# Kernel tuning notes

Hardware: AMD Instinct MI355X
Metric: run time of the kernel (lower is better)

## Reference

```python
import jax, jax.numpy as jnp
import numpy as np

N = 100000      # nodes
E = 1600000     # edges (avg degree 16)
DIN = 128       # input feature dim
DOUT = 64       # per-head output dim
H = 4           # independent heads, mean-aggregated
LRELU_ALPHA = 0.2  # tf.nn.leaky_relu default


def setup_inputs() -> dict:
    key = jax.random.key(0)
    k = jax.random.split(key, 7)
    inputs = jax.random.normal(k[0], (N, DIN), dtype=jnp.float32)
    edge_row = jnp.sort(jax.random.randint(k[1], (E,), 0, N, dtype=jnp.int32))
    edge_col = jax.random.randint(k[2], (E,), 0, N, dtype=jnp.int32)
    edge_val = jnp.ones((E,), dtype=jnp.float32)  # binary adjacency values
    # Glorot-ish scaled params per head
    W = jax.random.normal(k[3], (H, DIN, DOUT), dtype=jnp.float32) * np.float32(1.0 / np.sqrt(DIN))
    a1 = jax.random.normal(k[4], (H, DOUT), dtype=jnp.float32) * np.float32(1.0 / np.sqrt(DOUT))
    a2 = jax.random.normal(k[5], (H, DOUT), dtype=jnp.float32) * np.float32(1.0 / np.sqrt(DOUT))
    b = jnp.zeros((H, DOUT), dtype=jnp.float32)  # contrib.layers.bias_add bias
    return {"inputs": inputs, "W": W, "a1": a1, "a2": a2, "b": b,
            "edge_val": edge_val, "edge_row": edge_row, "edge_col": edge_col}


def _gat_head(inputs, Wh, a1h, a2h, bh, edge_val, edge_row, edge_col):
    xh = inputs @ Wh                          # [N, DOUT]  per-head projection
    f1 = jax.nn.elu(xh @ a1h)                 # [N]  Dense(D,1, act=elu) on key=x
    f2 = jax.nn.elu(xh @ a2h)                 # [N]
    # sparse_add of adj*f1 (row-broadcast) and adj*f2^T (col-broadcast)
    le = jax.nn.leaky_relu(edge_val * (f1[edge_row] + f2[edge_col]), LRELU_ALPHA)  # [E]
    # sparse softmax per destination row (reverse_axis=1)
    m = jax.ops.segment_max(le, edge_row, num_segments=N)        # [N]
    ex = jnp.exp(le - m[edge_row])                               # [E]
    s = jax.ops.segment_sum(ex, edge_row, num_segments=N)        # [N]
    coef = ex / s[edge_row]                                      # [E]
    # sparse_dense_matmul: out[r] = sum_e coef_e * x[col_e]
    out = jax.ops.segment_sum(coef[:, None] * xh[edge_col], edge_row, num_segments=N)  # [N, DOUT]
    return jax.nn.elu(out + bh)


def reference(inputs, W, a1, a2, b, edge_val, edge_row, edge_col):
    res = jnp.zeros((N, DOUT), dtype=inputs.dtype)
    for h in range(H):  # small fixed head count; each head has independent weights
        res = res + _gat_head(inputs, W[h], a1[h], a2[h], b[h], edge_val, edge_row, edge_col)
    return res / H
```

## Files before the change

### kernel.cpp

```cpp
#include <hip/hip_runtime.h>

#define NN 100000
#define EE 1600000
#define DIN 128
#define DOUT 64
#define NH 4

typedef __attribute__((ext_vector_type(8))) short bf16x8;
typedef __attribute__((ext_vector_type(4))) float f32x4;

__device__ __forceinline__ float elu_f(float x) {
  return x > 0.f ? x : (__expf(x) - 1.f);
}
__device__ __forceinline__ float lrelu_f(float x) {
  return x > 0.f ? x : 0.2f * x;
}
__device__ __forceinline__ float b2f(unsigned short u) {
  union { unsigned int i; float f; } v; v.i = ((unsigned int)u) << 16; return v.f;
}
__device__ __forceinline__ unsigned short f2b(float f) {
  union { float f; unsigned int i; } v; v.f = f;
  unsigned int r = v.i + 0x7fffu + ((v.i >> 16) & 1u);
  return (unsigned short)(r >> 16);
}

__global__ __launch_bounds__(256) void wbf_k(
    const float* __restrict__ W, unsigned short* __restrict__ wbt) {
  int idx = blockIdx.x * 256 + threadIdx.x;
  int col = idx >> 7, k = idx & 127;
  int h = col >> 6, j = col & 63;
  wbt[idx] = f2b(W[(size_t)h * DIN * DOUT + k * DOUT + j]);
}

__global__ __launch_bounds__(256) void build_row_ptr_k(
    const int* __restrict__ erow, int* __restrict__ rp) {
  int r = blockIdx.x * 256 + threadIdx.x;
  if (r > NN) return;
  int lo = 0, hi = EE;
  while (lo < hi) {
    int mid = (lo + hi) >> 1;
    if (erow[mid] < r) lo = mid + 1; else hi = mid;
  }
  rp[r] = lo;
}

__global__ __launch_bounds__(256) void proj_mfma_k(
    const float* __restrict__ inp, const unsigned short* __restrict__ wbt,
    const float* __restrict__ a1, const float* __restrict__ a2,
    float* __restrict__ f1p, float* __restrict__ f2p,
    unsigned short* __restrict__ xh) {
  const int tid = threadIdx.x;
  const int h = tid >> 6;
  const int l = tid & 63;
  const int lr = l & 15;
  const int lk = l >> 4;
  const int row0 = blockIdx.x * 64;

  bf16x8 bf[4][4];
  #pragma unroll
  for (int n = 0; n < 4; ++n) {
    const int col = h * DOUT + n * 16 + lr;
    #pragma unroll
    for (int kc = 0; kc < 4; ++kc)
      bf[n][kc] = *(const bf16x8*)(wbt + (size_t)col * DIN + kc * 32 + lk * 8);
  }

  f32x4 acc[4][4];
  #pragma unroll
  for (int m = 0; m < 4; ++m)
    #pragma unroll
    for (int n = 0; n < 4; ++n)
      acc[m][n] = (f32x4)(0.f);

  #pragma unroll
  for (int m = 0; m < 4; ++m) {
    int row = row0 + m * 16 + lr;
    int rowc = row < NN ? row : NN - 1;
    const float* ap = inp + (size_t)rowc * DIN;
    #pragma unroll
    for (int kc = 0; kc < 4; ++kc) {
      const float4 x0 = *(const float4*)(ap + kc * 32 + lk * 8);
      const float4 x1 = *(const float4*)(ap + kc * 32 + lk * 8 + 4);
      bf16x8 av;
      av[0] = (short)f2b(x0.x); av[1] = (short)f2b(x0.y);
      av[2] = (short)f2b(x0.z); av[3] = (short)f2b(x0.w);
      av[4] = (short)f2b(x1.x); av[5] = (short)f2b(x1.y);
      av[6] = (short)f2b(x1.z); av[7] = (short)f2b(x1.w);
      #pragma unroll
      for (int n = 0; n < 4; ++n)
        acc[m][n] = __builtin_amdgcn_mfma_f32_16x16x32_bf16(
            av, bf[n][kc], acc[m][n], 0, 0, 0);
    }
  }

  float a1v[4], a2v[4];
  #pragma unroll
  for (int n = 0; n < 4; ++n) {
    a1v[n] = a1[h * DOUT + n * 16 + lr];
    a2v[n] = a2[h * DOUT + n * 16 + lr];
  }

  #pragma unroll
  for (int m = 0; m < 4; ++m) {
    #pragma unroll
    for (int reg = 0; reg < 4; ++reg) {
      const int row = row0 + m * 16 + lk * 4 + reg;
      const bool ok = row < NN;
      float p1 = 0.f, p2 = 0.f;
      #pragma unroll
      for (int n = 0; n < 4; ++n) {
        const float v = acc[m][n][reg];
        if (ok)
          xh[(size_t)row * (NH * DOUT) + h * DOUT + n * 16 + lr] = f2b(v);
        p1 = fmaf(v, a1v[n], p1);
        p2 = fmaf(v, a2v[n], p2);
      }
      #pragma unroll
      for (int off = 1; off < 16; off <<= 1) {
        p1 += __shfl_xor(p1, off);
        p2 += __shfl_xor(p2, off);
      }
      if (ok && lr == 0) {
        f1p[(size_t)row * NH + h] = elu_f(p1);
        f2p[(size_t)row * NH + h] = elu_f(p2);
      }
    }
  }
}

__global__ __launch_bounds__(256) void agg_k(
    const int* __restrict__ rp, const int* __restrict__ ecol,
    const float* __restrict__ eval, const float* __restrict__ f1p,
    const float* __restrict__ f2p, const unsigned short* __restrict__ xh,
    const float* __restrict__ b, float* __restrict__ out) {
  const int tid = threadIdx.x;
  const int wave = tid >> 6, lane = tid & 63;
  const int r = blockIdx.x * 4 + wave;
  if (r >= NN) return;
  const int g = lane >> 4;
  int e0 = rp[r], e1 = rp[r + 1];
  e0 = __builtin_amdgcn_readfirstlane(e0);
  e1 = __builtin_amdgcn_readfirstlane(e1);
  const float f1r = f1p[(size_t)r * NH + g];
  float ax = 0.f, ay = 0.f, az = 0.f, aw = 0.f;
  float ssum = 0.f;
  int e = e0;
  for (; e + 4 <= e1; e += 4) {
    int c[4]; float vv[4];
    #pragma unroll
    for (int u = 0; u < 4; ++u) { c[u] = ecol[e + u]; vv[u] = eval[e + u]; }
    ushort4 xv[4]; float f2v[4];
    #pragma unroll
    for (int u = 0; u < 4; ++u) {
      xv[u] = *(const ushort4*)(xh + (size_t)c[u] * (NH * DOUT) + lane * 4);
      f2v[u] = f2p[(size_t)c[u] * NH + g];
    }
    #pragma unroll
    for (int u = 0; u < 4; ++u) {
      const float ex = __expf(lrelu_f(vv[u] * (f1r + f2v[u])));
      ssum += ex;
      ax = fmaf(ex, b2f(xv[u].x), ax);
      ay = fmaf(ex, b2f(xv[u].y), ay);
      az = fmaf(ex, b2f(xv[u].z), az);
      aw = fmaf(ex, b2f(xv[u].w), aw);
    }
  }
  for (; e < e1; ++e) {
    const int c = ecol[e];
    const float t = eval[e] * (f1r + f2p[(size_t)c * NH + g]);
    const float ex = __expf(lrelu_f(t));
    ssum += ex;
    const ushort4 xv = *(const ushort4*)(xh + (size_t)c * (NH * DOUT) + lane * 4);
    ax = fmaf(ex, b2f(xv.x), ax);
    ay = fmaf(ex, b2f(xv.y), ay);
    az = fmaf(ex, b2f(xv.z), az);
    aw = fmaf(ex, b2f(xv.w), aw);
  }
  const float4 bb = *(const float4*)(b + lane * 4);
  const float inv = (e1 > e0) ? (1.f / ssum) : 0.f;
  float v0 = elu_f(ax * inv + bb.x);
  float v1 = elu_f(ay * inv + bb.y);
  float v2 = elu_f(az * inv + bb.z);
  float v3 = elu_f(aw * inv + bb.w);
  v0 += __shfl_xor(v0, 16); v1 += __shfl_xor(v1, 16);
  v2 += __shfl_xor(v2, 16); v3 += __shfl_xor(v3, 16);
  v0 += __shfl_xor(v0, 32); v1 += __shfl_xor(v1, 32);
  v2 += __shfl_xor(v2, 32); v3 += __shfl_xor(v3, 32);
  if (lane < 16) {
    float4 o = make_float4(v0 * 0.25f, v1 * 0.25f, v2 * 0.25f, v3 * 0.25f);
    *(float4*)(out + (size_t)r * DOUT + lane * 4) = o;
  }
}

extern "C" void kernel_launch(void* const* d_in, const int* in_sizes, int n_in,
                              void* d_out, int out_size, void* d_ws, size_t ws_size,
                              hipStream_t stream) {
  const float* inp = (const float*)d_in[0];
  const float* W   = (const float*)d_in[1];
  const float* a1  = (const float*)d_in[2];
  const float* a2  = (const float*)d_in[3];
  const float* b   = (const float*)d_in[4];
  const float* ev  = (const float*)d_in[5];
  const int* erow  = (const int*)d_in[6];
  const int* ecol  = (const int*)d_in[7];
  float* out = (float*)d_out;

  char* ws = (char*)d_ws;
  size_t off = 0;
  int* rp = (int*)(ws + off);
  off += (((size_t)(NN + 1) * 4) + 255) & ~(size_t)255;
  float* f1p = (float*)(ws + off);
  off += (((size_t)NH * NN * 4) + 255) & ~(size_t)255;
  float* f2p = (float*)(ws + off);
  off += (((size_t)NH * NN * 4) + 255) & ~(size_t)255;
  unsigned short* xh = (unsigned short*)(ws + off);
  off += (((size_t)NN * NH * DOUT * 2) + 255) & ~(size_t)255;
  unsigned short* wbt = (unsigned short*)(ws + off);

  wbf_k<<<(NH * DIN * DOUT) / 256, 256, 0, stream>>>(W, wbt);
  build_row_ptr_k<<<(NN + 1 + 255) / 256, 256, 0, stream>>>(erow, rp);
  proj_mfma_k<<<(NN + 63) / 64, 256, 0, stream>>>(inp, wbt, a1, a2, f1p, f2p, xh);
  agg_k<<<(NN + 3) / 4, 256, 0, stream>>>(rp, ecol, ev, f1p, f2p, xh, b, out);
}
```

Baseline: 202.9 us.

## Stage projection inputs in swizzled LDS and unroll edge aggregation by eight

The projection kernel now converts each 64-row input tile to bf16 once into XOR-swizzled shared memory, rather than having all four head-waves reload and convert the same rows from global memory. It also swaps the MFMA operands so each lane holds four consecutive output columns, which allows packed ushort4 stores and a shorter shuffle reduction. The aggregation kernel unrolls the edge loop to eight and handles the remainder with a masked eight-wide batch so more gathers are in flight, and the output is written with nontemporal stores. In exchange the projection kernel uses 16 KB of LDS and a barrier, and the masked tail performs redundant loads.

```diff
diff --git a/kernel.cpp b/kernel.cpp
--- a/kernel.cpp
+++ b/kernel.cpp
@@ -49,6 +49,7 @@
     const float* __restrict__ a1, const float* __restrict__ a2,
     float* __restrict__ f1p, float* __restrict__ f2p,
     unsigned short* __restrict__ xh) {
+  __shared__ unsigned short lds_a[64 * 128];
   const int tid = threadIdx.x;
   const int h = tid >> 6;
   const int l = tid & 63;
@@ -56,6 +57,20 @@
   const int lk = l >> 4;
   const int row0 = blockIdx.x * 64;
 
+  #pragma unroll
+  for (int i = 0; i < 8; ++i) {
+    const int idx = i * 256 + tid;
+    const int row = idx >> 5;
+    const int c4 = idx & 31;
+    int grow = row0 + row;
+    if (grow >= NN) grow = NN - 1;
+    const float4 v = *(const float4*)(inp + (size_t)grow * DIN + c4 * 4);
+    ushort4 w;
+    w.x = f2b(v.x); w.y = f2b(v.y); w.z = f2b(v.z); w.w = f2b(v.w);
+    const int byte_off = row * 256 + ((c4 * 8) ^ ((row & 7) << 4));
+    *(ushort4*)((char*)lds_a + byte_off) = w;
+  }
+
   bf16x8 bf[4][4];
   #pragma unroll
   for (int n = 0; n < 4; ++n) {
@@ -64,6 +79,7 @@
     for (int kc = 0; kc < 4; ++kc)
       bf[n][kc] = *(const bf16x8*)(wbt + (size_t)col * DIN + kc * 32 + lk * 8);
   }
+  __syncthreads();
 
   f32x4 acc[4][4];
   #pragma unroll
@@ -74,56 +90,48 @@
 
   #pragma unroll
   for (int m = 0; m < 4; ++m) {
-    int row = row0 + m * 16 + lr;
-    int rowc = row < NN ? row : NN - 1;
-    const float* ap = inp + (size_t)rowc * DIN;
-    #pragma unroll
-    for (int kc = 0; kc < 4; ++kc) {
-      const float4 x0 = *(const float4*)(ap + kc * 32 + lk * 8);
-      const float4 x1 = *(const float4*)(ap + kc * 32 + lk * 8 + 4);
-      bf16x8 av;
-      av[0] = (short)f2b(x0.x); av[1] = (short)f2b(x0.y);
-      av[2] = (short)f2b(x0.z); av[3] = (short)f2b(x0.w);
-      av[4] = (short)f2b(x1.x); av[5] = (short)f2b(x1.y);
-      av[6] = (short)f2b(x1.z); av[7] = (short)f2b(x1.w);
+    const int r = m * 16 + lr;
+    bf16x8 af[4];
+    #pragma unroll
+    for (int kc = 0; kc < 4; ++kc)
+      af[kc] = *(const bf16x8*)((char*)lds_a + r * 256 +
+                                ((kc * 64 + lk * 16) ^ ((r & 7) << 4)));
+    #pragma unroll
+    for (int kc = 0; kc < 4; ++kc)
       #pragma unroll
       for (int n = 0; n < 4; ++n)
         acc[m][n] = __builtin_amdgcn_mfma_f32_16x16x32_bf16(
-            av, bf[n][kc], acc[m][n], 0, 0, 0);
-    }
-  }
-
-  float a1v[4], a2v[4];
+            bf[n][kc], af[kc], acc[m][n], 0, 0, 0);
+  }
+
+  float4 a1q[4], a2q[4];
   #pragma unroll
   for (int n = 0; n < 4; ++n) {
-    a1v[n] = a1[h * DOUT + n * 16 + lr];
-    a2v[n] = a2[h * DOUT + n * 16 + lr];
-  }
-
+    a1q[n] = *(const float4*)(a1 + h * DOUT + n * 16 + lk * 4);
+    a2q[n] = *(const float4*)(a2 + h * DOUT + n * 16 + lk * 4);
+  }
   #pragma unroll
   for (int m = 0; m < 4; ++m) {
-    #pragma unroll
-    for (int reg = 0; reg < 4; ++reg) {
-      const int row = row0 + m * 16 + lk * 4 + reg;
-      const bool ok = row < NN;
-      float p1 = 0.f, p2 = 0.f;
-      #pragma unroll
-      for (int n = 0; n < 4; ++n) {
-        const float v = acc[m][n][reg];
-        if (ok)
-          xh[(size_t)row * (NH * DOUT) + h * DOUT + n * 16 + lr] = f2b(v);
-        p1 = fmaf(v, a1v[n], p1);
-        p2 = fmaf(v, a2v[n], p2);
-      }
-      #pragma unroll
-      for (int off = 1; off < 16; off <<= 1) {
-        p1 += __shfl_xor(p1, off);
-        p2 += __shfl_xor(p2, off);
-      }
-      if (ok && lr == 0) {
-        f1p[(size_t)row * NH + h] = elu_f(p1);
-        f2p[(size_t)row * NH + h] = elu_f(p2);
-      }
+    const int row = row0 + m * 16 + lr;
+    const bool ok = row < NN;
+    float p1 = 0.f, p2 = 0.f;
+    #pragma unroll
+    for (int n = 0; n < 4; ++n) {
+      const f32x4 a = acc[m][n];
+      ushort4 pk;
+      pk.x = f2b(a[0]); pk.y = f2b(a[1]); pk.z = f2b(a[2]); pk.w = f2b(a[3]);
+      if (ok)
+        *(ushort4*)(xh + (size_t)row * (NH * DOUT) + h * DOUT + n * 16 + lk * 4) = pk;
+      p1 = fmaf(a[0], a1q[n].x, p1); p1 = fmaf(a[1], a1q[n].y, p1);
+      p1 = fmaf(a[2], a1q[n].z, p1); p1 = fmaf(a[3], a1q[n].w, p1);
+      p2 = fmaf(a[0], a2q[n].x, p2); p2 = fmaf(a[1], a2q[n].y, p2);
+      p2 = fmaf(a[2], a2q[n].z, p2); p2 = fmaf(a[3], a2q[n].w, p2);
+    }
+    p1 += __shfl_xor(p1, 16); p1 += __shfl_xor(p1, 32);
+    p2 += __shfl_xor(p2, 16); p2 += __shfl_xor(p2, 32);
+    if (ok && lk == 0) {
+      f1p[(size_t)row * NH + h] = elu_f(p1);
+      f2p[(size_t)row * NH + h] = elu_f(p2);
     }
   }
 }
@@ -138,25 +146,24 @@
   const int r = blockIdx.x * 4 + wave;
   if (r >= NN) return;
   const int g = lane >> 4;
-  int e0 = rp[r], e1 = rp[r + 1];
-  e0 = __builtin_amdgcn_readfirstlane(e0);
-  e1 = __builtin_amdgcn_readfirstlane(e1);
+  int e0 = __builtin_amdgcn_readfirstlane(rp[r]);
+  int e1 = __builtin_amdgcn_readfirstlane(rp[r + 1]);
   const float f1r = f1p[(size_t)r * NH + g];
   float ax = 0.f, ay = 0.f, az = 0.f, aw = 0.f;
   float ssum = 0.f;
   int e = e0;
-  for (; e + 4 <= e1; e += 4) {
-    int c[4]; float vv[4];
-    #pragma unroll
-    for (int u = 0; u < 4; ++u) { c[u] = ecol[e + u]; vv[u] = eval[e + u]; }
-    ushort4 xv[4]; float f2v[4];
-    #pragma unroll
-    for (int u = 0; u < 4; ++u) {
+  for (; e + 8 <= e1; e += 8) {
+    int c[8]; float vv[8];
+    #pragma unroll
+    for (int u = 0; u < 8; ++u) { c[u] = ecol[e + u]; vv[u] = eval[e + u]; }
+    ushort4 xv[8]; float f2v[8];
+    #pragma unroll
+    for (int u = 0; u < 8; ++u) {
       xv[u] = *(const ushort4*)(xh + (size_t)c[u] * (NH * DOUT) + lane * 4);
       f2v[u] = f2p[(size_t)c[u] * NH + g];
     }
     #pragma unroll
-    for (int u = 0; u < 4; ++u) {
+    for (int u = 0; u < 8; ++u) {
       const float ex = __expf(lrelu_f(vv[u] * (f1r + f2v[u])));
       ssum += ex;
       ax = fmaf(ex, b2f(xv[u].x), ax);
@@ -165,16 +172,31 @@
       aw = fmaf(ex, b2f(xv[u].w), aw);
     }
   }
-  for (; e < e1; ++e) {
-    const int c = ecol[e];
-    const float t = eval[e] * (f1r + f2p[(size_t)c * NH + g]);
-    const float ex = __expf(lrelu_f(t));
-    ssum += ex;
-    const ushort4 xv = *(const ushort4*)(xh + (size_t)c * (NH * DOUT) + lane * 4);
-    ax = fmaf(ex, b2f(xv.x), ax);
-    ay = fmaf(ex, b2f(xv.y), ay);
-    az = fmaf(ex, b2f(xv.z), az);
-    aw = fmaf(ex, b2f(xv.w), aw);
+  if (e < e1) {
+    int c[8]; float vv[8]; bool okk[8];
+    #pragma unroll
+    for (int u = 0; u < 8; ++u) {
+      int ee = e + u;
+      okk[u] = ee < e1;
+      if (!okk[u]) ee = e1 - 1;
+      c[u] = ecol[ee]; vv[u] = eval[ee];
+    }
+    ushort4 xv[8]; float f2v[8];
+    #pragma unroll
+    for (int u = 0; u < 8; ++u) {
+      xv[u] = *(const ushort4*)(xh + (size_t)c[u] * (NH * DOUT) + lane * 4);
+      f2v[u] = f2p[(size_t)c[u] * NH + g];
+    }
+    #pragma unroll
+    for (int u = 0; u < 8; ++u) {
+      float ex = __expf(lrelu_f(vv[u] * (f1r + f2v[u])));
+      ex = okk[u] ? ex : 0.f;
+      ssum += ex;
+      ax = fmaf(ex, b2f(xv[u].x), ax);
+      ay = fmaf(ex, b2f(xv[u].y), ay);
+      az = fmaf(ex, b2f(xv[u].z), az);
+      aw = fmaf(ex, b2f(xv[u].w), aw);
+    }
   }
   const float4 bb = *(const float4*)(b + lane * 4);
   const float inv = (e1 > e0) ? (1.f / ssum) : 0.f;
@@ -187,8 +209,8 @@
   v0 += __shfl_xor(v0, 32); v1 += __shfl_xor(v1, 32);
   v2 += __shfl_xor(v2, 32); v3 += __shfl_xor(v3, 32);
   if (lane < 16) {
-    float4 o = make_float4(v0 * 0.25f, v1 * 0.25f, v2 * 0.25f, v3 * 0.25f);
-    *(float4*)(out + (size_t)r * DOUT + lane * 4) = o;
+    f32x4 o = {v0 * 0.25f, v1 * 0.25f, v2 * 0.25f, v3 * 0.25f};
+    __builtin_nontemporal_store(o, (f32x4*)(out + (size_t)r * DOUT + lane * 4));
   }
 }
 
```

Result: faster. 177.2 us (-12.7%).
